# Performance work log

Hardware: AMD Instinct MI355X
Metric: run time of the kernel (lower is better)

Reference implementation:

```python
import jax, jax.numpy as jnp
import numpy as np

B, L, D, H = 2, 1024, 512, 8
h = D // H            # head_dim = 64
K = H                 # num_eigh must equal num_heads (vmap pairing in conv)
EPS = 1e-5


def _spectral_filters(seq_len: int, k: int) -> np.ndarray:
    # Hankel matrix Z_{ij} = 2 / ((i+j)^3 - (i+j)), top-k eigenvectors scaled by sigma^{1/4}
    e = np.arange(1, seq_len + 1, dtype=np.float64)
    ipj = e[:, None] + e[None, :]
    Z = 2.0 / (ipj ** 3 - ipj)
    sigma, phi = np.linalg.eigh(Z)
    sigma_k = np.clip(sigma[-k:], 1e-9, None)
    return (phi[:, -k:] * sigma_k ** 0.25).astype(np.float32)  # [L, K]


def setup_inputs() -> dict:
    key = jax.random.key(0)
    ks = jax.random.split(key, 8)
    s = 0.02
    return {
        "x": jax.random.normal(ks[0], (B, L, D), jnp.float32),
        "spectral_basis": jnp.asarray(_spectral_filters(L, K)),       # [L, K]
        "wq_w": jax.random.normal(ks[1], (D, D), jnp.float32) * s,
        "wq_b": jnp.zeros((D,), jnp.float32),
        "wk_w": jax.random.normal(ks[2], (D, D), jnp.float32) * s,
        "wk_b": jnp.zeros((D,), jnp.float32),
        "wv_w": jax.random.normal(ks[3], (D, D), jnp.float32) * s,
        "wv_b": jnp.zeros((D,), jnp.float32),
        "wo_w": jax.random.normal(ks[4], (D, D), jnp.float32) * s,
        "wo_b": jnp.zeros((D,), jnp.float32),
        "wg_w": jax.random.normal(ks[5], (h * h,), jnp.float32) * s,  # Linear(h^2 -> 1)
        "wg_b": jnp.zeros((), jnp.float32),
    }


def _causal_fft_conv(u, filt_f, n):
    # u: [B,H,L,h]; filt_f: precomputed rfft of per-head filters [H, F]
    Uf = jnp.fft.rfft(u, n=n, axis=2)                        # [B,H,F,h]
    y = jnp.fft.irfft(Uf * filt_f[None, :, :, None], n=n, axis=2)
    return y[:, :, :L]                                       # truncate full conv -> causal


def reference(x, spectral_basis, wq_w, wq_b, wk_w, wk_b, wv_w, wv_b,
              wo_w, wo_b, wg_w, wg_b):
    # projections -> [B,H,L,h]
    q = (x @ wq_w + wq_b).reshape(B, L, H, h).transpose(0, 2, 1, 3)
    k = (x @ wk_w + wk_b).reshape(B, L, H, h).transpose(0, 2, 1, 3) * h ** (-0.5)
    v = (x @ wv_w + wv_b).reshape(B, L, H, h).transpose(0, 2, 1, 3)

    n = 2 * L
    filt_f = jnp.fft.rfft(spectral_basis.T, n=n, axis=1)     # [H, F] (one filter per head)
    k_conv = _causal_fft_conv(k, filt_f, n)
    v_conv = _causal_fft_conv(v, filt_f, n)

    # gated outer product Z: [B,H,L,h,h]
    Z = jnp.einsum('bhlm,bhln->bhlmn', v_conv, k_conv)
    gate_logits = Z.reshape(B, H, L, h * h) @ wg_w + wg_b    # [B,H,L]
    gates = jax.nn.relu(gate_logits) ** 2 + EPS
    gated_Z = gates[..., None, None] * Z

    # associative scan (additive) over sequence dim
    cumul_gated_Z = jnp.cumsum(gated_Z, axis=2)              # [B,H,L,h,h]
    cumul_gates = jnp.cumsum(gates, axis=2)                  # [B,H,L]
    attn = cumul_gated_Z / (cumul_gates[..., None, None] + EPS)

    # note: original einsum sums over l (and d) independently of s
    ctxt = jnp.einsum('bhsd,bhlde->bhse', q, attn)           # [B,H,L,h]
    norm = jnp.linalg.norm(ctxt, axis=3, keepdims=True)
    unit = ctxt / jnp.maximum(norm, EPS)                     # F.normalize semantics
    out = unit.transpose(0, 2, 1, 3).reshape(B, L, D)
    return out @ wo_w + wo_b
```

## Files before the change

kernel.cpp:

```cpp
#include <hip/hip_runtime.h>
#include <math.h>


typedef __attribute__((ext_vector_type(8))) short short8;
typedef __attribute__((ext_vector_type(4))) float floatx4;

__device__ __forceinline__ unsigned short f2bf(float f) {
    unsigned int u = __float_as_uint(f);
    unsigned int r = (u + 0x7FFFu + ((u >> 16) & 1u)) >> 16;
    return (unsigned short)r;
}

__global__ __launch_bounds__(256) void k_prep(
    const float* __restrict__ x,
    const float* __restrict__ wq, const float* __restrict__ wk,
    const float* __restrict__ wv, const float* __restrict__ wo,
    const float* __restrict__ sb,
    unsigned short* __restrict__ xb,
    unsigned short* __restrict__ wT, unsigned short* __restrict__ woT,
    unsigned short* __restrict__ TB)
{
    __shared__ float sf[64][65];
    const int blk = blockIdx.x;
    const int tid = threadIdx.x;

    if (blk < 512) {
        const int gid = blk * 256 + tid;
        const float4* x4 = (const float4*)x;
        float4 a = x4[gid*2], b = x4[gid*2+1];
        uint4 o;
        o.x = f2bf(a.x) | ((unsigned)f2bf(a.y) << 16);
        o.y = f2bf(a.z) | ((unsigned)f2bf(a.w) << 16);
        o.z = f2bf(b.x) | ((unsigned)f2bf(b.y) << 16);
        o.w = f2bf(b.z) | ((unsigned)f2bf(b.w) << 16);
        ((uint4*)xb)[gid] = o;
    } else if (blk < 768) {
        const int t = blk - 512;
        const float* src; unsigned short* dst; int n0, c0, k0;
        if (t < 192) {
            int nt = t >> 3, kt = t & 7;
            n0 = nt * 64; k0 = kt * 64;
            int z = n0 >> 9; c0 = n0 & 511;
            src = (z == 0) ? wq : (z == 1) ? wk : wv;
            dst = wT;
        } else {
            int u = t - 192; int nt = u >> 3, kt = u & 7;
            n0 = nt * 64; c0 = n0; k0 = kt * 64;
            src = wo; dst = woT;
        }
        const int rr = tid >> 4, c4 = tid & 15;
        #pragma unroll
        for (int g = 0; g < 4; ++g) {
            int r = g*16 + rr;
            float4 v = *(const float4*)&src[(size_t)(k0 + r)*512 + c0 + c4*4];
            sf[r][c4*4+0]=v.x; sf[r][c4*4+1]=v.y; sf[r][c4*4+2]=v.z; sf[r][c4*4+3]=v.w;
        }
        __syncthreads();
        #pragma unroll
        for (int g = 0; g < 4; ++g) {
            int c = g*16 + rr;
            int kk = c4*4;
            ushort4 o;
            o.x = f2bf(sf[kk+0][c]); o.y = f2bf(sf[kk+1][c]);
            o.z = f2bf(sf[kk+2][c]); o.w = f2bf(sf[kk+3][c]);
            *(ushort4*)&dst[(size_t)(n0 + c)*512 + k0 + kk] = o;
        }
    } else {
        const int u = blk - 768;
        const int h = u >> 5;
        const int r0 = (u & 31) * 32;
        unsigned short* sbc = (unsigned short*)sf;
        for (int i = tid; i < 1024; i += 256)
            sbc[i] = f2bf(sb[i*8 + h]);
        __syncthreads();
        const int rr = tid >> 3, c0 = (tid & 7) * 128;
        const int t = r0 + rr;
        unsigned short* row = TB + ((size_t)h * 1024 + t) * 1024;
        for (int c = c0; c < c0 + 128; c += 8) {
            unsigned short v[8];
            #pragma unroll
            for (int j = 0; j < 8; ++j) {
                int s = c + j;
                v[j] = (t >= s) ? sbc[t - s] : (unsigned short)0;
            }
            uint4 o;
            o.x = v[0] | ((unsigned)v[1]<<16);
            o.y = v[2] | ((unsigned)v[3]<<16);
            o.z = v[4] | ((unsigned)v[5]<<16);
            o.w = v[6] | ((unsigned)v[7]<<16);
            *(uint4*)&row[c] = o;
        }
    }
}

__global__ __launch_bounds__(256) void k_qkv_mfma(
    const unsigned short* __restrict__ xb, const unsigned short* __restrict__ wT,
    const float* __restrict__ bq, const float* __restrict__ bk,
    const float* __restrict__ bv,
    float* __restrict__ qo, unsigned short* __restrict__ ub2)
{
    const int tid = threadIdx.x;
    const int lane = tid & 63, wave = tid >> 6;
    const int q = lane >> 4, ln = lane & 15;
    const int wm = (wave >> 1) * 64, wn = (wave & 1) * 64;
    const int m0 = blockIdx.y * 128;
    const int n0 = blockIdx.x * 128;

    __shared__ unsigned short As[128*40];
    __shared__ unsigned short Bs[128*40];

    floatx4 acc[4][4];
    #pragma unroll
    for (int i = 0; i < 4; ++i)
        #pragma unroll
        for (int j = 0; j < 4; ++j)
            acc[i][j] = (floatx4){0.f, 0.f, 0.f, 0.f};

    const uint4* Ag = (const uint4*)xb;
    const uint4* Bg = (const uint4*)wT;
    for (int k0 = 0; k0 < 512; k0 += 32) {
        #pragma unroll
        for (int s = 0; s < 2; ++s) {
            int c = tid*2 + s;
            int r = c >> 2, cp = c & 3;
            uint4 va = Ag[(size_t)(m0 + r)*64 + (k0 >> 3) + cp];
            uint4 vb = Bg[(size_t)(n0 + r)*64 + (k0 >> 3) + cp];
            *(uint4*)&As[r*40 + cp*8] = va;
            *(uint4*)&Bs[r*40 + cp*8] = vb;
        }
        __syncthreads();
        short8 af[4], bfr[4];
        #pragma unroll
        for (int i = 0; i < 4; ++i) {
            af[i]  = *(const short8*)&As[(wm + i*16 + ln)*40 + q*8];
            bfr[i] = *(const short8*)&Bs[(wn + i*16 + ln)*40 + q*8];
        }
        #pragma unroll
        for (int mi = 0; mi < 4; ++mi)
            #pragma unroll
            for (int ni = 0; ni < 4; ++ni)
                acc[mi][ni] = __builtin_amdgcn_mfma_f32_16x16x32_bf16(
                    af[mi], bfr[ni], acc[mi][ni], 0, 0, 0);
        __syncthreads();
    }

    const int z = n0 >> 9;
    if (z == 0) {
        #pragma unroll
        for (int mi = 0; mi < 4; ++mi) {
            #pragma unroll
            for (int ni = 0; ni < 4; ++ni) {
                int gcol = n0 + wn + ni*16 + ln;
                int c = gcol & 511;
                int head = c >> 6, dd = c & 63;
                float bb = bq[c];
                #pragma unroll
                for (int reg = 0; reg < 4; ++reg) {
                    int row = m0 + wm + mi*16 + q*4 + reg;
                    int b = row >> 10, l = row & 1023;
                    qo[(size_t)((b*8 + head)*1024 + l)*64 + dd] =
                        acc[mi][ni][reg] + bb;
                }
            }
        }
    } else {
        const float scale = (z == 1) ? 0.125f : 1.0f;
        const float* bias = (z == 1) ? bk : bv;
        unsigned short* dst = ub2 + (size_t)(z-1) * 16 * 64 * 1024;
        #pragma unroll
        for (int mi = 0; mi < 4; ++mi) {
            #pragma unroll
            for (int ni = 0; ni < 4; ++ni) {
                int gcol = n0 + wn + ni*16 + ln;
                int c = gcol & 511;
                int head = c >> 6, dd = c & 63;
                float bb = bias[c];
                int row0 = m0 + wm + mi*16 + q*4;
                int b = row0 >> 10, l0 = row0 & 1023;
                ushort4 o;
                o.x = f2bf((acc[mi][ni][0] + bb) * scale);
                o.y = f2bf((acc[mi][ni][1] + bb) * scale);
                o.z = f2bf((acc[mi][ni][2] + bb) * scale);
                o.w = f2bf((acc[mi][ni][3] + bb) * scale);
                *(ushort4*)&dst[((size_t)((b*8 + head)*64) + dd)*1024 + l0] = o;
            }
        }
    }
}

__global__ __launch_bounds__(256) void k_conv_mfma(
    const unsigned short* __restrict__ TB,
    const unsigned short* __restrict__ ub2,
    float* __restrict__ kc, float* __restrict__ vc)
{
    const int tid = threadIdx.x;
    const int lane = tid & 63, wave = tid >> 6;
    const int q = lane >> 4, ln = lane & 15;
    const int bht = blockIdx.x;
    const int it  = blockIdx.y;
    const int t0  = it * 64;
    const int bh  = bht & 15, h = bh & 7, tensor = bht >> 4;

    __shared__ unsigned short As[64*40];
    __shared__ unsigned short Bs[64*40];

    const uint4* Ag = (const uint4*)TB;
    const uint4* Bg = (const uint4*)ub2;
    const size_t abase = (size_t)h * 131072 + (size_t)t0 * 128;
    const size_t bbase = (size_t)bht * 8192;

    floatx4 acc[4];
    #pragma unroll
    for (int i = 0; i < 4; ++i) acc[i] = (floatx4){0.f,0.f,0.f,0.f};

    const int kend = t0 + 64;
    const int r = tid >> 2, cp = tid & 3;
    for (int k0 = 0; k0 < kend; k0 += 32) {
        uint4 va = Ag[abase + (size_t)r*128 + (k0 >> 3) + cp];
        uint4 vb = Bg[bbase + (size_t)r*128 + (k0 >> 3) + cp];
        *(uint4*)&As[r*40 + cp*8] = va;
        *(uint4*)&Bs[r*40 + cp*8] = vb;
        __syncthreads();
        short8 a = *(const short8*)&As[(wave*16 + ln)*40 + q*8];
        short8 b0 = *(const short8*)&Bs[(0*16 + ln)*40 + q*8];
        short8 b1 = *(const short8*)&Bs[(1*16 + ln)*40 + q*8];
        short8 b2 = *(const short8*)&Bs[(2*16 + ln)*40 + q*8];
        short8 b3 = *(const short8*)&Bs[(3*16 + ln)*40 + q*8];
        acc[0] = __builtin_amdgcn_mfma_f32_16x16x32_bf16(a, b0, acc[0], 0, 0, 0);
        acc[1] = __builtin_amdgcn_mfma_f32_16x16x32_bf16(a, b1, acc[1], 0, 0, 0);
        acc[2] = __builtin_amdgcn_mfma_f32_16x16x32_bf16(a, b2, acc[2], 0, 0, 0);
        acc[3] = __builtin_amdgcn_mfma_f32_16x16x32_bf16(a, b3, acc[3], 0, 0, 0);
        __syncthreads();
    }

    float* dst = (tensor ? vc : kc) + (size_t)bh * 65536;
    #pragma unroll
    for (int ni = 0; ni < 4; ++ni)
        #pragma unroll
        for (int reg = 0; reg < 4; ++reg) {
            int row = t0 + wave*16 + q*4 + reg;
            dst[(size_t)row*64 + ni*16 + ln] = acc[ni][reg];
        }
}

__global__ __launch_bounds__(256) void k_gate(
    const float* __restrict__ kc, const float* __restrict__ vc,
    const float* __restrict__ wg_w, const float* __restrict__ wg_b,
    float* __restrict__ gl)
{
    const int tid = threadIdx.x, tx = tid & 15, ty = tid >> 4;
    const int l0 = blockIdx.x * 64;
    const int bh = blockIdx.y;
    const float* kb = kc + (size_t)bh * 65536;
    const float* vb = vc + (size_t)bh * 65536;

    __shared__ float ks[64][17];
    __shared__ __align__(16) float wsh[16][68];
    float acc[4][4] = {};
    const float4* k4 = (const float4*)kb;
    for (int n0 = 0; n0 < 64; n0 += 16) {
        {
            int r = tid >> 2, c4 = tid & 3;
            float4 t = k4[(size_t)(l0 + r) * 16 + (n0 >> 2) + c4];
            ks[r][c4*4+0]=t.x; ks[r][c4*4+1]=t.y; ks[r][c4*4+2]=t.z; ks[r][c4*4+3]=t.w;
        }
        for (int i = tid; i < 1024; i += 256) {
            int r = i >> 6, c = i & 63;
            wsh[r][c] = wg_w[c*64 + n0 + r];
        }
        __syncthreads();
        #pragma unroll
        for (int kk = 0; kk < 16; ++kk) {
            float a[4];
            a[0] = ks[ty*4+0][kk]; a[1] = ks[ty*4+1][kk];
            a[2] = ks[ty*4+2][kk]; a[3] = ks[ty*4+3][kk];
            float4 b4 = *(const float4*)&wsh[kk][tx*4];
            float bb[4] = {b4.x, b4.y, b4.z, b4.w};
            #pragma unroll
            for (int ii = 0; ii < 4; ++ii)
                #pragma unroll
                for (int jj = 0; jj < 4; ++jj)
                    acc[ii][jj] += a[ii] * bb[jj];
        }
        __syncthreads();
    }
    __shared__ float red[64][17];
    const float wgb = wg_b[0];
    const float4* v4p = (const float4*)vb;
    #pragma unroll
    for (int i = 0; i < 4; ++i) {
        int lr = ty*4 + i;
        float4 vv = v4p[(size_t)(l0 + lr) * 16 + tx];
        red[lr][tx] = acc[i][0]*vv.x + acc[i][1]*vv.y + acc[i][2]*vv.z + acc[i][3]*vv.w;
    }
    __syncthreads();
    if (tid < 64) {
        float s = 0.0f;
        #pragma unroll
        for (int t = 0; t < 16; ++t) s += red[tid][t];
        float logit = s + wgb;
        float r = fmaxf(logit, 0.0f);
        gl[bh*1024 + l0 + tid] = r*r + 1e-5f;
    }
}

__global__ __launch_bounds__(256) void k_amat(
    const float* __restrict__ kc, const float* __restrict__ vc,
    const float* __restrict__ gl, float* __restrict__ apart)
{
    const int tid = threadIdx.x, tx = tid & 15, ty = tid >> 4;
    const int bh = blockIdx.x, slc = blockIdx.y;
    const float* kb = kc + (size_t)bh * 65536;
    const float* vb = vc + (size_t)bh * 65536;

    __shared__ float sbuf[256];
    __shared__ float wfull[1024];
    __shared__ __align__(16) float vs[16][68];
    __shared__ __align__(16) float ks2[16][68];

    {
        const float4 g4 = ((const float4*)(gl + bh*1024))[tid];
        float g[4] = {g4.x, g4.y, g4.z, g4.w};
        float p[4];
        p[0]=g[0]; p[1]=p[0]+g[1]; p[2]=p[1]+g[2]; p[3]=p[2]+g[3];
        const float s = p[3];
        sbuf[tid] = s;
        __syncthreads();
        for (int off = 1; off < 256; off <<= 1) {
            float t = (tid >= off) ? sbuf[tid-off] : 0.0f;
            __syncthreads();
            sbuf[tid] += t;
            __syncthreads();
        }
        const float base = sbuf[tid] - s;
        float r[4], pr[4];
        #pragma unroll
        for (int u = 0; u < 4; ++u) r[u] = 1.0f / (base + p[u] + 1e-5f);
        pr[0]=r[0]; pr[1]=pr[0]+r[1]; pr[2]=pr[1]+r[2]; pr[3]=pr[2]+r[3];
        const float sr = pr[3];
        __syncthreads();
        sbuf[tid] = sr;
        __syncthreads();
        for (int off = 1; off < 256; off <<= 1) {
            float t = (tid >= off) ? sbuf[tid-off] : 0.0f;
            __syncthreads();
            sbuf[tid] += t;
            __syncthreads();
        }
        const float Rtot  = sbuf[255];
        const float baser = sbuf[tid] - sr;
        wfull[tid*4+0] = g[0] * (Rtot - (baser + pr[0]) + r[0]);
        wfull[tid*4+1] = g[1] * (Rtot - (baser + pr[1]) + r[1]);
        wfull[tid*4+2] = g[2] * (Rtot - (baser + pr[2]) + r[2]);
        wfull[tid*4+3] = g[3] * (Rtot - (baser + pr[3]) + r[3]);
    }
    __syncthreads();

    float acc[4][4] = {};
    const float4* k4 = (const float4*)kb;
    const float4* v4 = (const float4*)vb;
    for (int j0 = slc*256; j0 < slc*256 + 256; j0 += 16) {
        {
            int r = tid >> 4, c4 = tid & 15;
            *(float4*)&vs[r][c4*4]  = v4[(size_t)(j0 + r)*16 + c4];
            *(float4*)&ks2[r][c4*4] = k4[(size_t)(j0 + r)*16 + c4];
        }
        __syncthreads();
        #pragma unroll
        for (int jj = 0; jj < 16; ++jj) {
            float wj = wfull[j0 + jj];
            float a[4];
            a[0] = vs[jj][ty*4+0]*wj; a[1] = vs[jj][ty*4+1]*wj;
            a[2] = vs[jj][ty*4+2]*wj; a[3] = vs[jj][ty*4+3]*wj;
            float4 b4 = *(const float4*)&ks2[jj][tx*4];
            float bb[4] = {b4.x, b4.y, b4.z, b4.w};
            #pragma unroll
            for (int ii = 0; ii < 4; ++ii)
                #pragma unroll
                for (int jc = 0; jc < 4; ++jc)
                    acc[ii][jc] += a[ii] * bb[jc];
        }
        __syncthreads();
    }
    float* ap = apart + (size_t)(slc*16 + bh) * 4096;
    #pragma unroll
    for (int i = 0; i < 4; ++i) {
        float4 o = { acc[i][0], acc[i][1], acc[i][2], acc[i][3] };
        *(float4*)&ap[(ty*4+i)*64 + tx*4] = o;
    }
}

__global__ __launch_bounds__(256) void k_ctxt(
    const float* __restrict__ q, const float* __restrict__ apart,
    unsigned short* __restrict__ ub)
{
    const int tid = threadIdx.x, tx = tid & 15, ty = tid >> 4;
    const int l0 = blockIdx.x * 64;
    const int bh = blockIdx.y;
    const float* qb = q + (size_t)bh * 65536;

    __shared__ float qs[64][17];
    __shared__ __align__(16) float As[16][68];
    float acc[4][4] = {};
    const float4* q4 = (const float4*)qb;
    const float4* a4 = (const float4*)apart;
    for (int d0 = 0; d0 < 64; d0 += 16) {
        {
            int r = tid >> 2, c4 = tid & 3;
            float4 t = q4[(size_t)(l0 + r)*16 + (d0 >> 2) + c4];
            qs[r][c4*4+0]=t.x; qs[r][c4*4+1]=t.y; qs[r][c4*4+2]=t.z; qs[r][c4*4+3]=t.w;
        }
        {
            int r = tid >> 4, c4 = tid & 15;
            size_t o = (size_t)(d0 + r)*16 + c4;
            float4 t0 = a4[(size_t)(0*16 + bh)*1024 + o];
            float4 t1 = a4[(size_t)(1*16 + bh)*1024 + o];
            float4 t2 = a4[(size_t)(2*16 + bh)*1024 + o];
            float4 t3 = a4[(size_t)(3*16 + bh)*1024 + o];
            float4 t;
            t.x = t0.x+t1.x+t2.x+t3.x; t.y = t0.y+t1.y+t2.y+t3.y;
            t.z = t0.z+t1.z+t2.z+t3.z; t.w = t0.w+t1.w+t2.w+t3.w;
            *(float4*)&As[r][c4*4] = t;
        }
        __syncthreads();
        #pragma unroll
        for (int dd = 0; dd < 16; ++dd) {
            float a[4];
            a[0] = qs[ty*4+0][dd]; a[1] = qs[ty*4+1][dd];
            a[2] = qs[ty*4+2][dd]; a[3] = qs[ty*4+3][dd];
            float4 b4 = *(const float4*)&As[dd][tx*4];
            float bb[4] = {b4.x, b4.y, b4.z, b4.w};
            #pragma unroll
            for (int ii = 0; ii < 4; ++ii)
                #pragma unroll
                for (int jj = 0; jj < 4; ++jj)
                    acc[ii][jj] += a[ii] * bb[jj];
        }
        __syncthreads();
    }
    __shared__ float red[64][17];
    __shared__ float nrm[64];
    #pragma unroll
    for (int i = 0; i < 4; ++i) {
        red[ty*4+i][tx] = acc[i][0]*acc[i][0] + acc[i][1]*acc[i][1]
                        + acc[i][2]*acc[i][2] + acc[i][3]*acc[i][3];
    }
    __syncthreads();
    if (tid < 64) {
        float s = 0.0f;
        #pragma unroll
        for (int t = 0; t < 16; ++t) s += red[tid][t];
        nrm[tid] = fmaxf(sqrtf(s), 1e-5f);
    }
    __syncthreads();
    const int b = bh >> 3, hd = bh & 7;
    #pragma unroll
    for (int i = 0; i < 4; ++i) {
        int lr = ty*4 + i;
        float inv = 1.0f / nrm[lr];
        ushort4 o;
        o.x = f2bf(acc[i][0]*inv); o.y = f2bf(acc[i][1]*inv);
        o.z = f2bf(acc[i][2]*inv); o.w = f2bf(acc[i][3]*inv);
        *(ushort4*)&ub[(size_t)(b*1024 + l0 + lr)*512 + hd*64 + tx*4] = o;
    }
}

__global__ __launch_bounds__(256) void k_out_mfma(
    const unsigned short* __restrict__ ub, const unsigned short* __restrict__ woT,
    const float* __restrict__ bo, float* __restrict__ out)
{
    const int tid = threadIdx.x;
    const int lane = tid & 63, wave = tid >> 6;
    const int q = lane >> 4, ln = lane & 15;
    const int wm = (wave >> 1) * 64, wn = (wave & 1) * 64;
    const int m0 = blockIdx.y * 128;
    const int n0 = blockIdx.x * 128;

    __shared__ unsigned short As[128*40];
    __shared__ unsigned short Bs[128*40];

    floatx4 acc[4][4];
    #pragma unroll
    for (int i = 0; i < 4; ++i)
        #pragma unroll
        for (int j = 0; j < 4; ++j)
            acc[i][j] = (floatx4){0.f, 0.f, 0.f, 0.f};

    const uint4* Ag = (const uint4*)ub;
    const uint4* Bg = (const uint4*)woT;
    for (int k0 = 0; k0 < 512; k0 += 32) {
        #pragma unroll
        for (int s = 0; s < 2; ++s) {
            int c = tid*2 + s;
            int r = c >> 2, cp = c & 3;
            uint4 va = Ag[(size_t)(m0 + r)*64 + (k0 >> 3) + cp];
            uint4 vb = Bg[(size_t)(n0 + r)*64 + (k0 >> 3) + cp];
            *(uint4*)&As[r*40 + cp*8] = va;
            *(uint4*)&Bs[r*40 + cp*8] = vb;
        }
        __syncthreads();
        short8 af[4], bfr[4];
        #pragma unroll
        for (int i = 0; i < 4; ++i) {
            af[i]  = *(const short8*)&As[(wm + i*16 + ln)*40 + q*8];
            bfr[i] = *(const short8*)&Bs[(wn + i*16 + ln)*40 + q*8];
        }
        #pragma unroll
        for (int mi = 0; mi < 4; ++mi)
            #pragma unroll
            for (int ni = 0; ni < 4; ++ni)
                acc[mi][ni] = __builtin_amdgcn_mfma_f32_16x16x32_bf16(
                    af[mi], bfr[ni], acc[mi][ni], 0, 0, 0);
        __syncthreads();
    }

    #pragma unroll
    for (int mi = 0; mi < 4; ++mi) {
        #pragma unroll
        for (int ni = 0; ni < 4; ++ni) {
            int gcol = n0 + wn + ni*16 + ln;
            float bb = bo[gcol];
            #pragma unroll
            for (int reg = 0; reg < 4; ++reg) {
                int row = m0 + wm + mi*16 + q*4 + reg;
                out[(size_t)row*512 + gcol] = acc[mi][ni][reg] + bb;
            }
        }
    }
}

extern "C" void kernel_launch(void* const* d_in, const int* in_sizes, int n_in,
                              void* d_out, int out_size, void* d_ws, size_t ws_size,
                              hipStream_t stream)
{
    const float* x   = (const float*)d_in[0];
    const float* sb  = (const float*)d_in[1];
    const float* wq  = (const float*)d_in[2];
    const float* bq  = (const float*)d_in[3];
    const float* wk  = (const float*)d_in[4];
    const float* bk  = (const float*)d_in[5];
    const float* wv  = (const float*)d_in[6];
    const float* bv  = (const float*)d_in[7];
    const float* wo  = (const float*)d_in[8];
    const float* bo  = (const float*)d_in[9];
    const float* wg  = (const float*)d_in[10];
    const float* wgb = (const float*)d_in[11];
    float* out = (float*)d_out;
    float* ws  = (float*)d_ws;

    float* Q   = ws;
    float* KC  = ws + 1048576;
    float* VC  = ws + 2*1048576;
    float* GL  = ws + 3*1048576;
    float* AP  = GL + 16384;
    float* fp  = AP + 262144;
    unsigned short* XB  = (unsigned short*)fp;
    unsigned short* WT  = XB  + 1048576;
    unsigned short* WOT = WT  + 786432;
    unsigned short* UB  = WOT + 262144;
    unsigned short* UB2 = UB  + 1048576;
    unsigned short* TB  = UB2 + 2097152;

    k_prep     <<<dim3(1024),   256, 0, stream>>>(x, wq, wk, wv, wo, sb,
                                                  XB, WT, WOT, TB);
    k_qkv_mfma <<<dim3(12, 16), 256, 0, stream>>>(XB, WT, bq, bk, bv, Q, UB2);
    k_conv_mfma<<<dim3(32, 16), 256, 0, stream>>>(TB, UB2, KC, VC);
    k_gate     <<<dim3(16, 16), 256, 0, stream>>>(KC, VC, wg, wgb, GL);
    k_amat     <<<dim3(16, 4),  256, 0, stream>>>(KC, VC, GL, AP);
    k_ctxt     <<<dim3(16, 16), 256, 0, stream>>>(Q, AP, UB);
    k_out_mfma <<<dim3(4, 16),  256, 0, stream>>>(UB, WOT, bo, out);
}
```

Measured before the change: 170.5 us.

## Fuse causal convolution and gate computation into one kernel

The k- and v-convolutions for one (batch, head, 64-row tile) now run in the same block, sharing the Toeplitz A tile, and the gate logits are computed right away from the results held in shared memory. This drops one kernel launch and the re-read of the conv outputs from global memory by the gate kernel. In exchange the grid is halved to 256 blocks, per-block shared memory grows a lot (gate weights plus k/v tiles, roughly 50KB), and the gate bilinear form runs as per-thread scalar FMAs that re-read the full weight matrix from LDS.

```diff
diff --git a/kernel.cpp b/kernel.cpp
--- a/kernel.cpp
+++ b/kernel.cpp
@@ -188,119 +188,106 @@
     }
 }
 
-__global__ __launch_bounds__(256) void k_conv_mfma(
+__global__ __launch_bounds__(256) void k_convgate(
     const unsigned short* __restrict__ TB,
     const unsigned short* __restrict__ ub2,
-    float* __restrict__ kc, float* __restrict__ vc)
+    const float* __restrict__ wg_w, const float* __restrict__ wg_b,
+    float* __restrict__ kc, float* __restrict__ vc, float* __restrict__ gl)
 {
     const int tid = threadIdx.x;
     const int lane = tid & 63, wave = tid >> 6;
     const int q = lane >> 4, ln = lane & 15;
-    const int bht = blockIdx.x;
-    const int it  = blockIdx.y;
-    const int t0  = it * 64;
-    const int bh  = bht & 15, h = bh & 7, tensor = bht >> 4;
+    const int it = blockIdx.x, t0 = it * 64;
+    const int bh = blockIdx.y, h = bh & 7;
 
     __shared__ unsigned short As[64*40];
-    __shared__ unsigned short Bs[64*40];
+    __shared__ unsigned short Bks[64*40];
+    __shared__ unsigned short Bvs[64*40];
+    __shared__ float wgs[4096];
+    __shared__ float kvt[2][64][68];
+    __shared__ float red[64][4];
+
+    for (int i = tid; i < 1024; i += 256)
+        ((float4*)wgs)[i] = ((const float4*)wg_w)[i];
 
     const uint4* Ag = (const uint4*)TB;
     const uint4* Bg = (const uint4*)ub2;
-    const size_t abase = (size_t)h * 131072 + (size_t)t0 * 128;
-    const size_t bbase = (size_t)bht * 8192;
-
-    floatx4 acc[4];
-    #pragma unroll
-    for (int i = 0; i < 4; ++i) acc[i] = (floatx4){0.f,0.f,0.f,0.f};
+    const size_t abase  = (size_t)h * 131072 + (size_t)t0 * 128;
+    const size_t bkbase = (size_t)bh * 8192;
+    const size_t bvbase = (size_t)(16 + bh) * 8192;
+
+    floatx4 acck[4], accv[4];
+    #pragma unroll
+    for (int i = 0; i < 4; ++i) {
+        acck[i] = (floatx4){0.f,0.f,0.f,0.f};
+        accv[i] = (floatx4){0.f,0.f,0.f,0.f};
+    }
 
     const int kend = t0 + 64;
     const int r = tid >> 2, cp = tid & 3;
     for (int k0 = 0; k0 < kend; k0 += 32) {
-        uint4 va = Ag[abase + (size_t)r*128 + (k0 >> 3) + cp];
-        uint4 vb = Bg[bbase + (size_t)r*128 + (k0 >> 3) + cp];
-        *(uint4*)&As[r*40 + cp*8] = va;
-        *(uint4*)&Bs[r*40 + cp*8] = vb;
+        uint4 va = Ag[abase  + (size_t)r*128 + (k0 >> 3) + cp];
+        uint4 vk = Bg[bkbase + (size_t)r*128 + (k0 >> 3) + cp];
+        uint4 vv = Bg[bvbase + (size_t)r*128 + (k0 >> 3) + cp];
+        *(uint4*)&As[r*40 + cp*8]  = va;
+        *(uint4*)&Bks[r*40 + cp*8] = vk;
+        *(uint4*)&Bvs[r*40 + cp*8] = vv;
         __syncthreads();
         short8 a = *(const short8*)&As[(wave*16 + ln)*40 + q*8];
-        short8 b0 = *(const short8*)&Bs[(0*16 + ln)*40 + q*8];
-        short8 b1 = *(const short8*)&Bs[(1*16 + ln)*40 + q*8];
-        short8 b2 = *(const short8*)&Bs[(2*16 + ln)*40 + q*8];
-        short8 b3 = *(const short8*)&Bs[(3*16 + ln)*40 + q*8];
-        acc[0] = __builtin_amdgcn_mfma_f32_16x16x32_bf16(a, b0, acc[0], 0, 0, 0);
-        acc[1] = __builtin_amdgcn_mfma_f32_16x16x32_bf16(a, b1, acc[1], 0, 0, 0);
-        acc[2] = __builtin_amdgcn_mfma_f32_16x16x32_bf16(a, b2, acc[2], 0, 0, 0);
-        acc[3] = __builtin_amdgcn_mfma_f32_16x16x32_bf16(a, b3, acc[3], 0, 0, 0);
-        __syncthreads();
-    }
-
-    float* dst = (tensor ? vc : kc) + (size_t)bh * 65536;
+        #pragma unroll
+        for (int ni = 0; ni < 4; ++ni) {
+            short8 bk8 = *(const short8*)&Bks[(ni*16 + ln)*40 + q*8];
+            short8 bv8 = *(const short8*)&Bvs[(ni*16 + ln)*40 + q*8];
+            acck[ni] = __builtin_amdgcn_mfma_f32_16x16x32_bf16(a, bk8, acck[ni], 0, 0, 0);
+            accv[ni] = __builtin_amdgcn_mfma_f32_16x16x32_bf16(a, bv8, accv[ni], 0, 0, 0);
+        }
+        __syncthreads();
+    }
+
+    float* dks = kc + (size_t)bh * 65536;
+    float* dvs = vc + (size_t)bh * 65536;
     #pragma unroll
     for (int ni = 0; ni < 4; ++ni)
         #pragma unroll
         for (int reg = 0; reg < 4; ++reg) {
-            int row = t0 + wave*16 + q*4 + reg;
-            dst[(size_t)row*64 + ni*16 + ln] = acc[ni][reg];
-        }
-}
-
-__global__ __launch_bounds__(256) void k_gate(
-    const float* __restrict__ kc, const float* __restrict__ vc,
-    const float* __restrict__ wg_w, const float* __restrict__ wg_b,
-    float* __restrict__ gl)
-{
-    const int tid = threadIdx.x, tx = tid & 15, ty = tid >> 4;
-    const int l0 = blockIdx.x * 64;
-    const int bh = blockIdx.y;
-    const float* kb = kc + (size_t)bh * 65536;
-    const float* vb = vc + (size_t)bh * 65536;
-
-    __shared__ float ks[64][17];
-    __shared__ __align__(16) float wsh[16][68];
-    float acc[4][4] = {};
-    const float4* k4 = (const float4*)kb;
-    for (int n0 = 0; n0 < 64; n0 += 16) {
-        {
-            int r = tid >> 2, c4 = tid & 3;
-            float4 t = k4[(size_t)(l0 + r) * 16 + (n0 >> 2) + c4];
-            ks[r][c4*4+0]=t.x; ks[r][c4*4+1]=t.y; ks[r][c4*4+2]=t.z; ks[r][c4*4+3]=t.w;
-        }
-        for (int i = tid; i < 1024; i += 256) {
-            int r = i >> 6, c = i & 63;
-            wsh[r][c] = wg_w[c*64 + n0 + r];
-        }
-        __syncthreads();
-        #pragma unroll
-        for (int kk = 0; kk < 16; ++kk) {
-            float a[4];
-            a[0] = ks[ty*4+0][kk]; a[1] = ks[ty*4+1][kk];
-            a[2] = ks[ty*4+2][kk]; a[3] = ks[ty*4+3][kk];
-            float4 b4 = *(const float4*)&wsh[kk][tx*4];
-            float bb[4] = {b4.x, b4.y, b4.z, b4.w};
-            #pragma unroll
-            for (int ii = 0; ii < 4; ++ii)
-                #pragma unroll
-                for (int jj = 0; jj < 4; ++jj)
-                    acc[ii][jj] += a[ii] * bb[jj];
-        }
-        __syncthreads();
-    }
-    __shared__ float red[64][17];
-    const float wgb = wg_b[0];
-    const float4* v4p = (const float4*)vb;
-    #pragma unroll
-    for (int i = 0; i < 4; ++i) {
-        int lr = ty*4 + i;
-        float4 vv = v4p[(size_t)(l0 + lr) * 16 + tx];
-        red[lr][tx] = acc[i][0]*vv.x + acc[i][1]*vv.y + acc[i][2]*vv.z + acc[i][3]*vv.w;
+            int row = wave*16 + q*4 + reg;
+            float kvv = acck[ni][reg];
+            float vvv = accv[ni][reg];
+            dks[(size_t)(t0 + row)*64 + ni*16 + ln] = kvv;
+            dvs[(size_t)(t0 + row)*64 + ni*16 + ln] = vvv;
+            kvt[0][row][ni*16 + ln] = kvv;
+            kvt[1][row][ni*16 + ln] = vvv;
+        }
+    __syncthreads();
+
+    {
+        const int row = tid >> 2, team = tid & 3;
+        float4 kreg[16];
+        #pragma unroll
+        for (int c = 0; c < 16; ++c)
+            kreg[c] = *(const float4*)&kvt[0][row][c*4];
+        float partial = 0.0f;
+        #pragma unroll
+        for (int mm = 0; mm < 16; ++mm) {
+            int m = team*16 + mm;
+            float vv = kvt[1][row][m];
+            float dot = 0.0f;
+            #pragma unroll
+            for (int c = 0; c < 16; ++c) {
+                float4 w4 = *(const float4*)&wgs[m*64 + c*4];
+                dot += w4.x*kreg[c].x + w4.y*kreg[c].y
+                     + w4.z*kreg[c].z + w4.w*kreg[c].w;
+            }
+            partial += vv * dot;
+        }
+        red[row][team] = partial;
     }
     __syncthreads();
     if (tid < 64) {
-        float s = 0.0f;
-        #pragma unroll
-        for (int t = 0; t < 16; ++t) s += red[tid][t];
-        float logit = s + wgb;
-        float r = fmaxf(logit, 0.0f);
-        gl[bh*1024 + l0 + tid] = r*r + 1e-5f;
+        float4 r4 = *(const float4*)&red[tid][0];
+        float s = r4.x + r4.y + r4.z + r4.w + wg_b[0];
+        float rr = fmaxf(s, 0.0f);
+        gl[bh*1024 + t0 + tid] = rr*rr + 1e-5f;
     }
 }
 
@@ -564,8 +551,7 @@
     k_prep     <<<dim3(1024),   256, 0, stream>>>(x, wq, wk, wv, wo, sb,
                                                   XB, WT, WOT, TB);
     k_qkv_mfma <<<dim3(12, 16), 256, 0, stream>>>(XB, WT, bq, bk, bv, Q, UB2);
-    k_conv_mfma<<<dim3(32, 16), 256, 0, stream>>>(TB, UB2, KC, VC);
-    k_gate     <<<dim3(16, 16), 256, 0, stream>>>(KC, VC, wg, wgb, GL);
+    k_convgate <<<dim3(16, 16), 256, 0, stream>>>(TB, UB2, wg, wgb, KC, VC, GL);
     k_amat     <<<dim3(16, 4),  256, 0, stream>>>(KC, VC, GL, AP);
     k_ctxt     <<<dim3(16, 16), 256, 0, stream>>>(Q, AP, UB);
     k_out_mfma <<<dim3(4, 16),  256, 0, stream>>>(UB, WOT, bo, out);
```

Result: slower. 175.4 us (+2.8%).
